# Kernel optimization log

Hardware: AMD Instinct MI355X
Metric: run time of the kernel (lower is better)

## Reference

```python
import jax, jax.numpy as jnp
import numpy as np

B, S, HID = 2, 2048, 2048
H, D_NOPE, D_ROPE, D_V, R = 16, 128, 64, 128, 512
D_Q = D_NOPE + D_ROPE  # 192
MAX_POS = 4096
EPS = 1e-6


def setup_inputs() -> dict:
    key = jax.random.key(0)
    ks = jax.random.split(key, 10)
    hidden_states = jax.random.normal(ks[0], (B, S, HID), dtype=jnp.float32)
    cos = jax.random.uniform(ks[1], (MAX_POS, D_ROPE // 2), dtype=jnp.float32)
    sin = jax.random.uniform(ks[2], (MAX_POS, D_ROPE // 2), dtype=jnp.float32)
    position_ids = jnp.arange(B * S, dtype=jnp.int64).reshape(B, S)
    sc = lambda d: 1.0 / np.sqrt(d)
    Wq = jax.random.normal(ks[3], (HID, H * D_Q), dtype=jnp.float32) * sc(HID)
    Wkv_a = jax.random.normal(ks[4], (HID, R + D_ROPE), dtype=jnp.float32) * sc(HID)
    ln_g = jnp.ones((R,), dtype=jnp.float32)
    ln_b = jnp.zeros((R,), dtype=jnp.float32)
    Wkv_b = jax.random.normal(ks[5], (R, H * (D_NOPE + D_V)), dtype=jnp.float32) * sc(R)
    Wo = jax.random.normal(ks[6], (H * D_V, HID), dtype=jnp.float32) * sc(H * D_V)
    return {"hidden_states": hidden_states, "cos": cos, "sin": sin,
            "position_ids": position_ids, "Wq": Wq, "Wkv_a": Wkv_a,
            "ln_g": ln_g, "ln_b": ln_b, "Wkv_b": Wkv_b, "Wo": Wo}


def _rope(t, cos, sin, position_ids):
    # t: [B,S,Hh,D_ROPE]; cos/sin: [MAX_POS, D_ROPE//2]
    c = cos[position_ids]  # [B,S,D_ROPE//2]
    s = sin[position_ids]
    c2 = jnp.concatenate([c, c], axis=-1)[:, :, None, :]  # [B,S,1,D_ROPE]
    s2 = jnp.concatenate([s, s], axis=-1)[:, :, None, :]
    half = t.shape[-1] // 2
    x1, x2 = t[..., :half], t[..., half:]
    rot = jnp.concatenate([-x2, x1], axis=-1)
    return t * c2 + rot * s2


def reference(hidden_states, cos, sin, position_ids, Wq, Wkv_a, ln_g, ln_b, Wkv_b, Wo):
    b, s, _ = hidden_states.shape
    # Q projection -> split nope/rope parts
    q = (hidden_states @ Wq).reshape(b, s, H, D_Q)
    q_nope, q_pe = q[..., :D_NOPE], q[..., D_NOPE:]
    q_pe = _rope(q_pe, cos, sin, position_ids)
    query = jnp.concatenate([q_nope, q_pe], axis=-1)  # [B,S,H,192]

    # KV latent projection
    ckv = hidden_states @ Wkv_a  # [B,S,R+D_ROPE]
    kv_c, k_pe = ckv[..., :R], ckv[..., R:]
    mu = jnp.mean(kv_c, axis=-1, keepdims=True)
    var = jnp.mean(jnp.square(kv_c - mu), axis=-1, keepdims=True)
    kv_c_n = (kv_c - mu) * jax.lax.rsqrt(var + EPS) * ln_g + ln_b
    k_pe = _rope(k_pe[:, :, None, :], cos, sin, position_ids)[:, :, 0, :]  # [B,S,64]

    # Expand latent -> per-head k_nope / v
    kv = (kv_c_n @ Wkv_b).reshape(b, s, H, D_NOPE + D_V)
    k_nope, v = kv[..., :D_NOPE], kv[..., D_NOPE:]
    key = jnp.concatenate(
        [k_nope, jnp.broadcast_to(k_pe[:, :, None, :], (b, s, H, D_ROPE))], axis=-1)

    scale = D_Q ** -0.5
    scores = jnp.einsum('bqhd,bkhd->bhqk', query, key) * scale
    causal = jnp.tril(jnp.ones((s, s), dtype=bool))
    scores = jnp.where(causal[None, None], scores, jnp.finfo(scores.dtype).min)
    attn = jax.nn.softmax(scores, axis=-1)
    out = jnp.einsum('bhqk,bkhd->bqhd', attn, v).reshape(b, s, H * D_V)
    return out @ Wo
```

## Files before the change

### kernel.cpp

```cpp
#include <hip/hip_runtime.h>
#include <math.h>
#include <stdint.h>

#define B_      2
#define S_      2048
#define HID_    2048
#define H_      16
#define D_NOPE_ 128
#define D_ROPE_ 64
#define D_V_    128
#define R_      512
#define D_Q_    192
#define NTOK    (B_ * S_)
#define EPS_    1e-6f

typedef __attribute__((ext_vector_type(8))) short bf16x8;
typedef __attribute__((ext_vector_type(4))) float f32x4;

__device__ __forceinline__ short f2bf(float x) {
    union { float f; unsigned u; } un; un.f = x;
    unsigned r = (un.u + 0x7fffu + ((un.u >> 16) & 1u)) >> 16;
    return (short)r;
}
__device__ __forceinline__ float bf2f(short s) {
    union { unsigned u; float f; } un;
    un.u = ((unsigned)(unsigned short)s) << 16;
    return un.f;
}

__device__ __forceinline__ void async_ld16(const short* gsrc, short* ldst) {
    __builtin_amdgcn_global_load_lds(
        (const __attribute__((address_space(1))) void*)gsrc,
        (__attribute__((address_space(3))) void*)ldst, 16, 0, 0);
}

#define BARX() { __builtin_amdgcn_sched_barrier(0); __builtin_amdgcn_s_barrier(); __builtin_amdgcn_sched_barrier(0); }

__device__ __forceinline__ void tc_body(const float* __restrict__ W,
                                        short* __restrict__ WT,
                                        int K, int Nreal, int bx, int by, int t) {
    __shared__ float T[32][33];
    const int n0 = bx * 32, k0 = by * 32;
    const int r = t >> 3, c4 = (t & 7) * 4;
    float4 v = make_float4(0.f, 0.f, 0.f, 0.f);
    if (n0 < Nreal) v = *(const float4*)&W[(size_t)(k0 + r) * Nreal + n0 + c4];
    T[r][c4 + 0] = v.x; T[r][c4 + 1] = v.y; T[r][c4 + 2] = v.z; T[r][c4 + 3] = v.w;
    __syncthreads();
    const int n = t >> 3, k4 = (t & 7) * 4;
    ushort4 o;
    o.x = (unsigned short)f2bf(T[k4 + 0][n]);
    o.y = (unsigned short)f2bf(T[k4 + 1][n]);
    o.z = (unsigned short)f2bf(T[k4 + 2][n]);
    o.w = (unsigned short)f2bf(T[k4 + 3][n]);
    *(ushort4*)&WT[(size_t)(n0 + n) * K + k0 + k4] = o;
}

__global__ __launch_bounds__(256) void prep(const float* __restrict__ hidden,
                                            short* __restrict__ hid_bf,
                                            const float* __restrict__ Wq,
                                            const float* __restrict__ Wkv_a,
                                            const float* __restrict__ Wkv_b,
                                            const float* __restrict__ Wo,
                                            short* __restrict__ WqkaT,
                                            short* __restrict__ WkbT,
                                            short* __restrict__ WoT) {
    const int bid = blockIdx.x, t = threadIdx.x;
    if (bid < 8192) {
        int i = bid * 256 + t;
        float4 v = ((const float4*)hidden)[i];
        ushort4 o;
        o.x = (unsigned short)f2bf(v.x); o.y = (unsigned short)f2bf(v.y);
        o.z = (unsigned short)f2bf(v.z); o.w = (unsigned short)f2bf(v.w);
        ((ushort4*)hid_bf)[i] = o;
    } else if (bid < 8192 + 6144) {
        int idx = bid - 8192;
        tc_body(Wq, WqkaT, 2048, 3072, idx % 96, idx / 96, t);
    } else if (bid < 8192 + 6144 + 1536) {
        int idx = bid - (8192 + 6144);
        tc_body(Wkv_a, WqkaT + (size_t)3072 * 2048, 2048, 576, idx % 24, idx / 24, t);
    } else if (bid < 8192 + 6144 + 1536 + 2048) {
        int idx = bid - (8192 + 6144 + 1536);
        tc_body(Wkv_b, WkbT, 512, 4096, idx % 128, idx / 128, t);
    } else {
        int idx = bid - (8192 + 6144 + 1536 + 2048);
        tc_body(Wo, WoT, 2048, 2048, idx % 64, idx / 64, t);
    }
}

template <int QA>
__global__ __launch_bounds__(512) void gemm8(const short* __restrict__ A,
                                             const short* __restrict__ BT,
                                             void* __restrict__ C0,
                                             float* __restrict__ C1,
                                             short* __restrict__ VtOut,
                                             const float* __restrict__ cosT,
                                             const float* __restrict__ sinT,
                                             const int* __restrict__ pid,
                                             int N, int K, int nbx) {
    __shared__ short LB[2][4][8192];

    const int tid = threadIdx.x, lane = tid & 63, w = tid >> 6;
    const int c16 = lane & 15, g = lane >> 4;
    const int wr = w >> 2, wc = w & 3;
    const int qph = (g ^ ((c16 >> 1) & 3)) * 8;

    const int nwg = gridDim.x;
    const int swz = (blockIdx.x & 7) * (nwg >> 3) + (blockIdx.x >> 3);
    const int brow = (swz / nbx) * 256, bcol = (swz % nbx) * 256;

    const int o0 = w * 1024 + lane * 16;
    const int o1 = o0 + 8192;
    const int r0 = o0 >> 6, lc0 = ((o0 >> 4) & 3) ^ ((r0 >> 1) & 3);
    const int r1 = o1 >> 6, lc1 = ((o1 >> 4) & 3) ^ ((r1 >> 1) & 3);
    const short* aS0 = A + (size_t)(brow + r0) * K + lc0 * 8;
    const short* aS1 = A + (size_t)(brow + r1) * K + lc1 * 8;
    const short* bS0 = BT + (size_t)(bcol + r0) * K + lc0 * 8;
    const short* bS1 = BT + (size_t)(bcol + r1) * K + lc1 * 8;
    const int d0 = w * 512, d1 = 4096 + w * 512;

    f32x4 zero = {0.f, 0.f, 0.f, 0.f};
    f32x4 acc[8][4];
#pragma unroll
    for (int i = 0; i < 8; ++i)
#pragma unroll
        for (int j = 0; j < 4; ++j) acc[i][j] = zero;

    const int NT = K >> 6;
    async_ld16(aS0,      &LB[0][0][d0]);  async_ld16(aS1,      &LB[0][0][d1]);
    async_ld16(aS0 + 32, &LB[0][1][d0]);  async_ld16(aS1 + 32, &LB[0][1][d1]);
    async_ld16(bS0,      &LB[0][2][d0]);  async_ld16(bS1,      &LB[0][2][d1]);
    async_ld16(bS0 + 32, &LB[0][3][d0]);  async_ld16(bS1 + 32, &LB[0][3][d1]);
    asm volatile("s_waitcnt vmcnt(0)" ::: "memory");
    BARX();

    int cur = 0;
    const int arb = wr * 128, brb = wc * 64;
    for (int kt = 0; kt < NT; ++kt) {
        const bool stg = (kt + 1 < NT);
        const int ko = (kt + 1) * 64;
        short (*CB)[8192] = LB[cur];
        short (*NB)[8192] = LB[cur ^ 1];
        bf16x8 af[4], bf[4];

#pragma unroll
        for (int ni = 0; ni < 4; ++ni)
            bf[ni] = *(const bf16x8*)&CB[2][(brb + ni * 16 + c16) * 32 + qph];
#pragma unroll
        for (int mi = 0; mi < 4; ++mi)
            af[mi] = *(const bf16x8*)&CB[0][(arb + mi * 16 + c16) * 32 + qph];
        if (stg) { async_ld16(aS0 + ko, &NB[0][d0]); async_ld16(aS1 + ko, &NB[0][d1]); }
        BARX();
        __builtin_amdgcn_s_setprio(1);
#pragma unroll
        for (int mi = 0; mi < 4; ++mi)
#pragma unroll
            for (int ni = 0; ni < 4; ++ni)
                acc[mi][ni] = __builtin_amdgcn_mfma_f32_16x16x32_bf16(af[mi], bf[ni], acc[mi][ni], 0, 0, 0);
        __builtin_amdgcn_s_setprio(0);
        BARX();

#pragma unroll
        for (int mi = 0; mi < 4; ++mi)
            af[mi] = *(const bf16x8*)&CB[0][(arb + 64 + mi * 16 + c16) * 32 + qph];
        if (stg) {
            async_ld16(bS0 + ko, &NB[2][d0]); async_ld16(bS1 + ko, &NB[2][d1]);
            asm volatile("s_waitcnt vmcnt(4)" ::: "memory");
        } else {
            asm volatile("s_waitcnt vmcnt(0)" ::: "memory");
        }
        BARX();
        __builtin_amdgcn_s_setprio(1);
#pragma unroll
        for (int mi = 0; mi < 4; ++mi)
#pragma unroll
            for (int ni = 0; ni < 4; ++ni)
                acc[4 + mi][ni] = __builtin_amdgcn_mfma_f32_16x16x32_bf16(af[mi], bf[ni], acc[4 + mi][ni], 0, 0, 0);
        __builtin_amdgcn_s_setprio(0);
        BARX();

#pragma unroll
        for (int ni = 0; ni < 4; ++ni)
            bf[ni] = *(const bf16x8*)&CB[3][(brb + ni * 16 + c16) * 32 + qph];
#pragma unroll
        for (int mi = 0; mi < 4; ++mi)
            af[mi] = *(const bf16x8*)&CB[1][(arb + mi * 16 + c16) * 32 + qph];
        if (stg) { async_ld16(aS0 + ko + 32, &NB[1][d0]); async_ld16(aS1 + ko + 32, &NB[1][d1]); }
        BARX();
        __builtin_amdgcn_s_setprio(1);
#pragma unroll
        for (int mi = 0; mi < 4; ++mi)
#pragma unroll
            for (int ni = 0; ni < 4; ++ni)
                acc[mi][ni] = __builtin_amdgcn_mfma_f32_16x16x32_bf16(af[mi], bf[ni], acc[mi][ni], 0, 0, 0);
        __builtin_amdgcn_s_setprio(0);
        BARX();

#pragma unroll
        for (int mi = 0; mi < 4; ++mi)
            af[mi] = *(const bf16x8*)&CB[1][(arb + 64 + mi * 16 + c16) * 32 + qph];
        if (stg) {
            async_ld16(bS0 + ko + 32, &NB[3][d0]); async_ld16(bS1 + ko + 32, &NB[3][d1]);
            asm volatile("s_waitcnt vmcnt(4)" ::: "memory");
        }
        BARX();
        __builtin_amdgcn_s_setprio(1);
#pragma unroll
        for (int mi = 0; mi < 4; ++mi)
#pragma unroll
            for (int ni = 0; ni < 4; ++ni)
                acc[4 + mi][ni] = __builtin_amdgcn_mfma_f32_16x16x32_bf16(af[mi], bf[ni], acc[4 + mi][ni], 0, 0, 0);
        __builtin_amdgcn_s_setprio(0);
        BARX();

        cur ^= 1;
    }

    if (QA) {
        const int wcol = bcol + wc * 64;
        if (wcol < 3072) {
            short* qb = (short*)C0;
            if ((wcol % 192) == 128) {
#pragma unroll
                for (int mi = 0; mi < 8; ++mi)
#pragma unroll
                    for (int reg = 0; reg < 4; ++reg) {
                        int row = brow + wr * 128 + mi * 16 + 4 * g + reg;
                        int pos = pid[row];
                        float cc1 = cosT[pos * 32 + c16],      ss1 = sinT[pos * 32 + c16];
                        float cc2 = cosT[pos * 32 + 16 + c16], ss2 = sinT[pos * 32 + 16 + c16];
                        float a0 = acc[mi][0][reg], a1 = acc[mi][1][reg];
                        float a2 = acc[mi][2][reg], a3 = acc[mi][3][reg];
                        size_t rb = (size_t)row * 3072 + wcol;
                        qb[rb + c16]      = f2bf(a0 * cc1 - a2 * ss1);
                        qb[rb + 16 + c16] = f2bf(a1 * cc2 - a3 * ss2);
                        qb[rb + 32 + c16] = f2bf(a2 * cc1 + a0 * ss1);
                        qb[rb + 48 + c16] = f2bf(a3 * cc2 + a1 * ss2);
                    }
            } else {
#pragma unroll
                for (int mi = 0; mi < 8; ++mi)
#pragma unroll
                    for (int ni = 0; ni < 4; ++ni)
#pragma unroll
                        for (int reg = 0; reg < 4; ++reg) {
                            int row = brow + wr * 128 + mi * 16 + 4 * g + reg;
                            qb[(size_t)row * 3072 + wcol + ni * 16 + c16] = f2bf(acc[mi][ni][reg]);
                        }
            }
        } else if (wcol < 3712) {
#pragma unroll
            for (int mi = 0; mi < 8; ++mi)
#pragma unroll
                for (int ni = 0; ni < 4; ++ni)
#pragma unroll
                    for (int reg = 0; reg < 4; ++reg) {
                        int row = brow + wr * 128 + mi * 16 + 4 * g + reg;
                        int col = wcol - 3072 + ni * 16 + c16;
                        C1[(size_t)row * 640 + col] = acc[mi][ni][reg];
                    }
        }
    } else {
        short* cc = (short*)C0;
        short* LT = &LB[0][0][0];
        const int wcol = bcol + wc * 64;
        if (wc < 2) {
#pragma unroll
            for (int mi = 0; mi < 8; ++mi)
#pragma unroll
                for (int ni = 0; ni < 4; ++ni)
#pragma unroll
                    for (int reg = 0; reg < 4; ++reg) {
                        int row = brow + wr * 128 + mi * 16 + 4 * g + reg;
                        cc[(size_t)row * N + wcol + ni * 16 + c16] = f2bf(acc[mi][ni][reg]);
                    }
        } else {
#pragma unroll
            for (int mi = 0; mi < 8; ++mi)
#pragma unroll
                for (int ni = 0; ni < 4; ++ni)
#pragma unroll
                    for (int reg = 0; reg < 4; ++reg) {
                        int d = wc * 64 - 128 + ni * 16 + c16;
                        int s = wr * 128 + mi * 16 + 4 * g + reg;
                        LT[d * 256 + (s ^ ((d & 15) << 3))] = f2bf(acc[mi][ni][reg]);
                    }
        }
        __syncthreads();
        const int bb = brow >> 11, hh = bcol >> 8, sbase = brow & 2047;
#pragma unroll
        for (int j = 0; j < 8; ++j) {
            int d = j * 16 + (tid >> 5);
            int s0 = (tid & 31) * 8;
            bf16x8 v = *(const bf16x8*)&LT[d * 256 + (s0 ^ ((d & 15) << 3))];
            *(bf16x8*)&VtOut[((size_t)((bb * 16 + hh) * 128 + d)) * 2048 + sbase + s0] = v;
        }
    }
}

__global__ __launch_bounds__(512) void gemm8n(const short* __restrict__ A,
                                              const short* __restrict__ BT,
                                              float* __restrict__ C,
                                              int N, int K, int nbx) {
    __shared__ short LA[2][2][4096];
    __shared__ short LBt[2][2][8192];

    const int tid = threadIdx.x, lane = tid & 63, w = tid >> 6;
    const int c16 = lane & 15, g = lane >> 4;
    const int wr = w >> 2, wc = w & 3;
    const int qph = (g ^ ((c16 >> 1) & 3)) * 8;

    const int nwg = gridDim.x;
    const int swz = (blockIdx.x & 7) * (nwg >> 3) + (blockIdx.x >> 3);
    const int brow = (swz / nbx) * 128, bcol = (swz % nbx) * 256;

    const int oA = tid * 16;
    const int rA = oA >> 6, lcA = ((oA >> 4) & 3) ^ ((rA >> 1) & 3);
    const short* aS = A + (size_t)(brow + rA) * K + lcA * 8;
    const int dA = oA >> 1;

    const int o0 = w * 1024 + lane * 16, o1 = o0 + 8192;
    const int r0 = o0 >> 6, lc0 = ((o0 >> 4) & 3) ^ ((r0 >> 1) & 3);
    const int r1 = o1 >> 6, lc1 = ((o1 >> 4) & 3) ^ ((r1 >> 1) & 3);
    const short* bS0 = BT + (size_t)(bcol + r0) * K + lc0 * 8;
    const short* bS1 = BT + (size_t)(bcol + r1) * K + lc1 * 8;
    const int d0 = o0 >> 1, d1 = o1 >> 1;

    f32x4 zero = {0.f, 0.f, 0.f, 0.f};
    f32x4 acc[4][4];
#pragma unroll
    for (int i = 0; i < 4; ++i)
#pragma unroll
        for (int j = 0; j < 4; ++j) acc[i][j] = zero;

    const int NT = K >> 6;
    async_ld16(aS,      &LA[0][0][dA]);
    async_ld16(aS + 32, &LA[0][1][dA]);
    async_ld16(bS0,      &LBt[0][0][d0]); async_ld16(bS1,      &LBt[0][0][d1]);
    async_ld16(bS0 + 32, &LBt[0][1][d0]); async_ld16(bS1 + 32, &LBt[0][1][d1]);
    asm volatile("s_waitcnt vmcnt(0)" ::: "memory");
    BARX();

    int cur = 0;
    const int arb = wr * 64, brb = wc * 64;
    for (int kt = 0; kt < NT; ++kt) {
        const bool stg = (kt + 1 < NT);
        const int ko = (kt + 1) * 64;
        bf16x8 af[4], bf[4];

#pragma unroll
        for (int mi = 0; mi < 4; ++mi)
            af[mi] = *(const bf16x8*)&LA[cur][0][(arb + mi * 16 + c16) * 32 + qph];
#pragma unroll
        for (int ni = 0; ni < 4; ++ni)
            bf[ni] = *(const bf16x8*)&LBt[cur][0][(brb + ni * 16 + c16) * 32 + qph];
        if (stg) {
            async_ld16(aS + ko, &LA[cur ^ 1][0][dA]);
            async_ld16(bS0 + ko, &LBt[cur ^ 1][0][d0]);
            async_ld16(bS1 + ko, &LBt[cur ^ 1][0][d1]);
            asm volatile("s_waitcnt vmcnt(3)" ::: "memory");
        } else {
            asm volatile("s_waitcnt vmcnt(0)" ::: "memory");
        }
        BARX();
        __builtin_amdgcn_s_setprio(1);
#pragma unroll
        for (int mi = 0; mi < 4; ++mi)
#pragma unroll
            for (int ni = 0; ni < 4; ++ni)
                acc[mi][ni] = __builtin_amdgcn_mfma_f32_16x16x32_bf16(af[mi], bf[ni], acc[mi][ni], 0, 0, 0);
        __builtin_amdgcn_s_setprio(0);
        BARX();

#pragma unroll
        for (int mi = 0; mi < 4; ++mi)
            af[mi] = *(const bf16x8*)&LA[cur][1][(arb + mi * 16 + c16) * 32 + qph];
#pragma unroll
        for (int ni = 0; ni < 4; ++ni)
            bf[ni] = *(const bf16x8*)&LBt[cur][1][(brb + ni * 16 + c16) * 32 + qph];
        if (stg) {
            async_ld16(aS + ko + 32, &LA[cur ^ 1][1][dA]);
            async_ld16(bS0 + ko + 32, &LBt[cur ^ 1][1][d0]);
            async_ld16(bS1 + ko + 32, &LBt[cur ^ 1][1][d1]);
            asm volatile("s_waitcnt vmcnt(3)" ::: "memory");
        }
        BARX();
        __builtin_amdgcn_s_setprio(1);
#pragma unroll
        for (int mi = 0; mi < 4; ++mi)
#pragma unroll
            for (int ni = 0; ni < 4; ++ni)
                acc[mi][ni] = __builtin_amdgcn_mfma_f32_16x16x32_bf16(af[mi], bf[ni], acc[mi][ni], 0, 0, 0);
        __builtin_amdgcn_s_setprio(0);
        BARX();

        cur ^= 1;
    }

#pragma unroll
    for (int mi = 0; mi < 4; ++mi)
#pragma unroll
        for (int ni = 0; ni < 4; ++ni)
#pragma unroll
            for (int reg = 0; reg < 4; ++reg) {
                int row = brow + wr * 64 + mi * 16 + 4 * g + reg;
                int col = bcol + wc * 64 + ni * 16 + c16;
                C[(size_t)row * N + col] = acc[mi][ni][reg];
            }
}

__global__ __launch_bounds__(256) void ln_rope(const float* __restrict__ ckv,
                                               const float* __restrict__ gam,
                                               const float* __restrict__ bet,
                                               const float* __restrict__ cosT,
                                               const float* __restrict__ sinT,
                                               const int* __restrict__ pid,
                                               short* __restrict__ kvcn,
                                               short* __restrict__ kpe) {
    const int tok = blockIdx.x, tid = threadIdx.x;
    const float* x = ckv + (size_t)tok * 640;
    float v0 = x[tid], v1 = x[tid + 256];
    float s = v0 + v1, sq = v0 * v0 + v1 * v1;
#pragma unroll
    for (int m = 1; m < 64; m <<= 1) { s += __shfl_xor(s, m); sq += __shfl_xor(sq, m); }
    __shared__ float ws[8];
    int wid = tid >> 6, lane = tid & 63;
    if (lane == 0) { ws[wid] = s; ws[4 + wid] = sq; }
    __syncthreads();
    s = ws[0] + ws[1] + ws[2] + ws[3];
    sq = ws[4] + ws[5] + ws[6] + ws[7];
    float mean = s * (1.f / 512.f);
    float var = sq * (1.f / 512.f) - mean * mean;
    float rstd = rsqrtf(var + EPS_);
    kvcn[(size_t)tok * 512 + tid]       = f2bf((v0 - mean) * rstd * gam[tid] + bet[tid]);
    kvcn[(size_t)tok * 512 + tid + 256] = f2bf((v1 - mean) * rstd * gam[tid + 256] + bet[tid + 256]);
    if (tid < 32) {
        int pos = pid[tok];
        float c = cosT[pos * 32 + tid], sn = sinT[pos * 32 + tid];
        float x1 = x[512 + tid], x2 = x[512 + 32 + tid];
        kpe[(size_t)tok * 64 + tid]      = f2bf(x1 * c - x2 * sn);
        kpe[(size_t)tok * 64 + 32 + tid] = f2bf(x2 * c + x1 * sn);
    }
}

__global__ __launch_bounds__(256) void flash_mfma(const short* __restrict__ qb,
                                                  const short* __restrict__ kvb,
                                                  const short* __restrict__ kpe,
                                                  const short* __restrict__ Vt,
                                                  short* __restrict__ attno) {
    __shared__ short Ks[2][64 * 128];
    __shared__ short Vs[2][128 * 64];
    __shared__ short P[4][16][72];

    const int flat = blockIdx.x;
    const int xcd = flat & 7, idx = flat >> 3;
    const int bh = xcd + 8 * (idx >> 4);
    const int pair = idx & 15;
    const int b = bh >> 4, h = bh & 15;

    const int tid = threadIdx.x, lane = tid & 63, w = tid >> 6;
    const int c16 = lane & 15, g = lane >> 4, g8 = g * 8;
    const float SC2 = 0.10412063f;

    const int o = w * 1024 + lane * 16;
    const int rK = o >> 8, ccK = ((o >> 4) & 15) ^ (rK & 7);
    const int rV = o >> 7, ccV = ((o >> 4) & 7) ^ (rV & 7);
    const short* kB0  = kvb + ((size_t)((b * 2048 + rK) * 16 + h)) * 256 + ccK * 8;
    const short* vB0  = Vt + ((size_t)((b * 16 + h) * 128 + rV)) * 2048 + ccV * 8;
    const short* peB0 = kpe + (size_t)(b * 2048 + c16) * 64 + g8;

    f32x4 zero = {0.f, 0.f, 0.f, 0.f};

#define STAGE(BUF)                                                                  \
    {                                                                               \
        _Pragma("unroll")                                                           \
        for (int rnd = 0; rnd < 4; ++rnd)                                           \
            async_ld16(kRun + (size_t)rnd * 65536,                                  \
                       &Ks[BUF][(rnd * 4096 + w * 1024) >> 1]);                     \
        _Pragma("unroll")                                                           \
        for (int rnd = 0; rnd < 4; ++rnd)                                           \
            async_ld16(vRun + (size_t)rnd * 65536,                                  \
                       &Vs[BUF][(rnd * 4096 + w * 1024) >> 1]);                     \
        kRun += 64 * 4096;                                                          \
        vRun += 64;                                                                 \
    }

    for (int half = 0; half < 2; ++half) {
        const int qt = half ? (31 - pair) : pair;
        const int q0 = qt * 64;
        const int qrow = q0 + w * 16;

        const size_t qbase = ((size_t)(b * 2048 + qrow + c16) * 16 + h) * 192 + g8;
        bf16x8 qf[6];
#pragma unroll
        for (int ks = 0; ks < 6; ++ks) qf[ks] = *(const bf16x8*)(qb + qbase + 32 * ks);

        f32x4 acc[8];
#pragma unroll
        for (int i = 0; i < 8; ++i) acc[i] = zero;
        float mreg = -INFINITY;
        float lreg = 0.f;

        const short* kRun = kB0;
        const short* vRun = vB0;
        const short* peRun = peB0;

        const int nt = qt + 1;
        STAGE(0);
        __syncthreads();
        int cur = 0;

        for (int kt = 0; kt < nt; ++kt) {
            if (kt + 1 < nt) STAGE(cur ^ 1);

            f32x4 sc[4];
#pragma unroll
            for (int i = 0; i < 4; ++i) sc[i] = zero;

            __builtin_amdgcn_s_setprio(1);
#pragma unroll
            for (int ks = 0; ks < 4; ++ks)
#pragma unroll
                for (int nb = 0; nb < 4; ++nb) {
                    int row = nb * 16 + c16;
                    bf16x8 kf = *(const bf16x8*)&Ks[cur][row * 128 + (((g + 4 * ks) ^ (row & 7)) << 3)];
                    sc[nb] = __builtin_amdgcn_mfma_f32_16x16x32_bf16(kf, qf[ks], sc[nb], 0, 0, 0);
                }
#pragma unroll
            for (int ks = 0; ks < 2; ++ks)
#pragma unroll
                for (int nb = 0; nb < 4; ++nb) {
                    bf16x8 kf = *(const bf16x8*)(peRun + (size_t)nb * 16 * 64 + ks * 32);
                    sc[nb] = __builtin_amdgcn_mfma_f32_16x16x32_bf16(kf, qf[4 + ks], sc[nb], 0, 0, 0);
                }
            __builtin_amdgcn_s_setprio(0);
            peRun += 64 * 64;

            if (kt == nt - 1) {
#pragma unroll
                for (int nb = 0; nb < 4; ++nb)
#pragma unroll
                    for (int reg = 0; reg < 4; ++reg)
                        if (nb * 16 + 4 * g + reg > w * 16 + c16) sc[nb][reg] = -INFINITY;
            }

            float m01 = fmaxf(fmaxf(sc[0][0], sc[0][1]), fmaxf(sc[0][2], sc[0][3]));
            float m23 = fmaxf(fmaxf(sc[1][0], sc[1][1]), fmaxf(sc[1][2], sc[1][3]));
            float m45 = fmaxf(fmaxf(sc[2][0], sc[2][1]), fmaxf(sc[2][2], sc[2][3]));
            float m67 = fmaxf(fmaxf(sc[3][0], sc[3][1]), fmaxf(sc[3][2], sc[3][3]));
            float rmax = fmaxf(fmaxf(m01, m23), fmaxf(m45, m67));
            rmax = fmaxf(rmax, __shfl_xor(rmax, 16));
            rmax = fmaxf(rmax, __shfl_xor(rmax, 32));

            if (__any(rmax * SC2 - mreg > 8.f)) {
                float mnew = fmaxf(mreg, rmax * SC2);
                float alpha = exp2f(mreg - mnew);
                mreg = mnew;
                lreg *= alpha;
                float ar[4];
#pragma unroll
                for (int reg = 0; reg < 4; ++reg) ar[reg] = __shfl(alpha, 4 * g + reg);
#pragma unroll
                for (int nb = 0; nb < 8; ++nb)
#pragma unroll
                    for (int reg = 0; reg < 4; ++reg) acc[nb][reg] *= ar[reg];
            }

#pragma unroll
            for (int nb = 0; nb < 4; ++nb) {
                float p0 = exp2f(fmaf(sc[nb][0], SC2, -mreg));
                float p1 = exp2f(fmaf(sc[nb][1], SC2, -mreg));
                float p2 = exp2f(fmaf(sc[nb][2], SC2, -mreg));
                float p3 = exp2f(fmaf(sc[nb][3], SC2, -mreg));
                lreg += (p0 + p1) + (p2 + p3);
                short* pr = &P[w][c16][nb * 16 + 4 * g];
                pr[0] = f2bf(p0); pr[1] = f2bf(p1); pr[2] = f2bf(p2); pr[3] = f2bf(p3);
            }

            __builtin_amdgcn_s_setprio(1);
#pragma unroll
            for (int ks = 0; ks < 2; ++ks) {
                bf16x8 pf = *(const bf16x8*)&P[w][c16][ks * 32 + g8];
#pragma unroll
                for (int nb = 0; nb < 8; ++nb) {
                    int row = nb * 16 + c16;
                    bf16x8 vf = *(const bf16x8*)&Vs[cur][row * 64 + (((g + 4 * ks) ^ (row & 7)) << 3)];
                    acc[nb] = __builtin_amdgcn_mfma_f32_16x16x32_bf16(pf, vf, acc[nb], 0, 0, 0);
                }
            }
            __builtin_amdgcn_s_setprio(0);

            __syncthreads();
            cur ^= 1;
        }

        lreg += __shfl_xor(lreg, 16);
        lreg += __shfl_xor(lreg, 32);
        float linv[4];
#pragma unroll
        for (int reg = 0; reg < 4; ++reg) linv[reg] = 1.f / __shfl(lreg, 4 * g + reg);
#pragma unroll
        for (int nb = 0; nb < 8; ++nb)
#pragma unroll
            for (int reg = 0; reg < 4; ++reg)
                attno[((size_t)(b * 2048 + qrow + 4 * g + reg) * 16 + h) * 128 + nb * 16 + c16] =
                    f2bf(acc[nb][reg] * linv[reg]);
    }
#undef STAGE
}

extern "C" void kernel_launch(void* const* d_in, const int* in_sizes, int n_in,
                              void* d_out, int out_size, void* d_ws, size_t ws_size,
                              hipStream_t stream) {
    const float* hidden = (const float*)d_in[0];
    const float* cosT   = (const float*)d_in[1];
    const float* sinT   = (const float*)d_in[2];
    const int*   pid    = (const int*)d_in[3];
    const float* Wq     = (const float*)d_in[4];
    const float* Wkv_a  = (const float*)d_in[5];
    const float* ln_g   = (const float*)d_in[6];
    const float* ln_b   = (const float*)d_in[7];
    const float* Wkv_b  = (const float*)d_in[8];
    const float* Wo     = (const float*)d_in[9];
    float* out = (float*)d_out;

    char* p = (char*)d_ws;
    short* hid_bf = (short*)p;               p += (size_t)NTOK * 2048 * 2;
    short* WqkaT  = (short*)p;               p += (size_t)3840 * 2048 * 2;
    short* WkbT   = (short*)p;               p += (size_t)4096 * 512 * 2;
    short* WoT    = (short*)p;               p += (size_t)2048 * 2048 * 2;
    char*  big    = p;                       p += (size_t)NTOK * 3072 * 4;
    short* qbuf   = (short*)p;               p += (size_t)NTOK * 3072 * 2;
    short* kvcn   = (short*)p;               p += (size_t)NTOK * 512 * 2;
    short* kpe    = (short*)p;               p += (size_t)NTOK * 64 * 2;
    short* kvb    = (short*)p;               p += (size_t)NTOK * 4096 * 2;

    float* ckv   = (float*)big;
    short* Vt    = (short*)(big + (size_t)NTOK * 640 * 4);
    short* attno = (short*)(big + (size_t)NTOK * 640 * 4 + (size_t)2 * 16 * 128 * 2048 * 2);

    prep<<<22016, 256, 0, stream>>>(hidden, hid_bf, Wq, Wkv_a, Wkv_b, Wo, WqkaT, WkbT, WoT);
    gemm8<1><<<240, 512, 0, stream>>>(hid_bf, WqkaT, qbuf, ckv, nullptr,
                                      cosT, sinT, pid, 3840, 2048, 15);
    ln_rope<<<NTOK, 256, 0, stream>>>(ckv, ln_g, ln_b, cosT, sinT, pid, kvcn, kpe);
    gemm8<0><<<256, 512, 0, stream>>>(kvcn, WkbT, kvb, nullptr, Vt,
                                      nullptr, nullptr, nullptr, 4096, 512, 16);
    flash_mfma<<<512, 256, 0, stream>>>(qbuf, kvb, kpe, Vt, attno);
    gemm8n<<<256, 512, 0, stream>>>(attno, WoT, out, 2048, 2048, 8);
}
```

Measured before the change: 274.4 us.

## Single-buffer flash attention LDS with split K/V staging and one q-tile per block

The flash attention kernel drops double-buffered K/V shared memory in favour of single buffers. K for the next tile is staged right after the QK^T phase and V after the PV phase, with extra barriers between them. Each block now handles one 64-row query tile (1024 blocks, heaviest tiles first) instead of a balanced pair of tiles. Launch bounds request 3 blocks per CU. The goal is higher occupancy and better latency hiding, at the cost of less load/compute overlap inside a block and more per-block setup.

```diff
diff --git a/kernel.cpp b/kernel.cpp
--- a/kernel.cpp
+++ b/kernel.cpp
@@ -442,20 +442,21 @@
     }
 }
 
-__global__ __launch_bounds__(256) void flash_mfma(const short* __restrict__ qb,
-                                                  const short* __restrict__ kvb,
-                                                  const short* __restrict__ kpe,
-                                                  const short* __restrict__ Vt,
-                                                  short* __restrict__ attno) {
-    __shared__ short Ks[2][64 * 128];
-    __shared__ short Vs[2][128 * 64];
+__global__ __launch_bounds__(256, 3) void flash_mfma(const short* __restrict__ qb,
+                                                     const short* __restrict__ kvb,
+                                                     const short* __restrict__ kpe,
+                                                     const short* __restrict__ Vt,
+                                                     short* __restrict__ attno) {
+    __shared__ short Ks[64 * 128];
+    __shared__ short Vs[128 * 64];
     __shared__ short P[4][16][72];
 
     const int flat = blockIdx.x;
     const int xcd = flat & 7, idx = flat >> 3;
-    const int bh = xcd + 8 * (idx >> 4);
-    const int pair = idx & 15;
+    const int bh = xcd + 8 * (idx >> 5);
+    const int qt = 31 - (idx & 31);
     const int b = bh >> 4, h = bh & 15;
+    const int q0 = qt * 64;
 
     const int tid = threadIdx.x, lane = tid & 63, w = tid >> 6;
     const int c16 = lane & 15, g = lane >> 4, g8 = g * 8;
@@ -464,148 +465,145 @@
     const int o = w * 1024 + lane * 16;
     const int rK = o >> 8, ccK = ((o >> 4) & 15) ^ (rK & 7);
     const int rV = o >> 7, ccV = ((o >> 4) & 7) ^ (rV & 7);
-    const short* kB0  = kvb + ((size_t)((b * 2048 + rK) * 16 + h)) * 256 + ccK * 8;
-    const short* vB0  = Vt + ((size_t)((b * 16 + h) * 128 + rV)) * 2048 + ccV * 8;
-    const short* peB0 = kpe + (size_t)(b * 2048 + c16) * 64 + g8;
+    const short* kRun = kvb + ((size_t)((b * 2048 + rK) * 16 + h)) * 256 + ccK * 8;
+    const short* vRun = Vt + ((size_t)((b * 16 + h) * 128 + rV)) * 2048 + ccV * 8;
+    const short* peRun = kpe + (size_t)(b * 2048 + c16) * 64 + g8;
+
+    const int qrow = q0 + w * 16;
+    const size_t qbase = ((size_t)(b * 2048 + qrow + c16) * 16 + h) * 192 + g8;
+    bf16x8 qf[6];
+#pragma unroll
+    for (int ks = 0; ks < 6; ++ks) qf[ks] = *(const bf16x8*)(qb + qbase + 32 * ks);
 
     f32x4 zero = {0.f, 0.f, 0.f, 0.f};
-
-#define STAGE(BUF)                                                                  \
+    f32x4 acc[8];
+#pragma unroll
+    for (int i = 0; i < 8; ++i) acc[i] = zero;
+    float mreg = -INFINITY;
+    float lreg = 0.f;
+
+#define STAGE_K()                                                                   \
     {                                                                               \
         _Pragma("unroll")                                                           \
         for (int rnd = 0; rnd < 4; ++rnd)                                           \
             async_ld16(kRun + (size_t)rnd * 65536,                                  \
-                       &Ks[BUF][(rnd * 4096 + w * 1024) >> 1]);                     \
+                       &Ks[(rnd * 4096 + w * 1024) >> 1]);                          \
+        kRun += 64 * 4096;                                                          \
+    }
+#define STAGE_V()                                                                   \
+    {                                                                               \
         _Pragma("unroll")                                                           \
         for (int rnd = 0; rnd < 4; ++rnd)                                           \
             async_ld16(vRun + (size_t)rnd * 65536,                                  \
-                       &Vs[BUF][(rnd * 4096 + w * 1024) >> 1]);                     \
-        kRun += 64 * 4096;                                                          \
+                       &Vs[(rnd * 4096 + w * 1024) >> 1]);                          \
         vRun += 64;                                                                 \
     }
 
-    for (int half = 0; half < 2; ++half) {
-        const int qt = half ? (31 - pair) : pair;
-        const int q0 = qt * 64;
-        const int qrow = q0 + w * 16;
-
-        const size_t qbase = ((size_t)(b * 2048 + qrow + c16) * 16 + h) * 192 + g8;
-        bf16x8 qf[6];
-#pragma unroll
-        for (int ks = 0; ks < 6; ++ks) qf[ks] = *(const bf16x8*)(qb + qbase + 32 * ks);
-
-        f32x4 acc[8];
-#pragma unroll
-        for (int i = 0; i < 8; ++i) acc[i] = zero;
-        float mreg = -INFINITY;
-        float lreg = 0.f;
-
-        const short* kRun = kB0;
-        const short* vRun = vB0;
-        const short* peRun = peB0;
-
-        const int nt = qt + 1;
-        STAGE(0);
+    const int nt = qt + 1;
+    STAGE_K();
+    STAGE_V();
+    __syncthreads();
+
+    for (int kt = 0; kt < nt; ++kt) {
+        const bool stg = (kt + 1 < nt);
+
+        f32x4 sc[4];
+#pragma unroll
+        for (int i = 0; i < 4; ++i) sc[i] = zero;
+
+        __builtin_amdgcn_s_setprio(1);
+#pragma unroll
+        for (int ks = 0; ks < 4; ++ks)
+#pragma unroll
+            for (int nb = 0; nb < 4; ++nb) {
+                int row = nb * 16 + c16;
+                bf16x8 kf = *(const bf16x8*)&Ks[row * 128 + (((g + 4 * ks) ^ (row & 7)) << 3)];
+                sc[nb] = __builtin_amdgcn_mfma_f32_16x16x32_bf16(kf, qf[ks], sc[nb], 0, 0, 0);
+            }
+#pragma unroll
+        for (int ks = 0; ks < 2; ++ks)
+#pragma unroll
+            for (int nb = 0; nb < 4; ++nb) {
+                bf16x8 kf = *(const bf16x8*)(peRun + (size_t)nb * 16 * 64 + ks * 32);
+                sc[nb] = __builtin_amdgcn_mfma_f32_16x16x32_bf16(kf, qf[4 + ks], sc[nb], 0, 0, 0);
+            }
+        __builtin_amdgcn_s_setprio(0);
+        peRun += 64 * 64;
+
         __syncthreads();
-        int cur = 0;
-
-        for (int kt = 0; kt < nt; ++kt) {
-            if (kt + 1 < nt) STAGE(cur ^ 1);
-
-            f32x4 sc[4];
-#pragma unroll
-            for (int i = 0; i < 4; ++i) sc[i] = zero;
-
-            __builtin_amdgcn_s_setprio(1);
-#pragma unroll
-            for (int ks = 0; ks < 4; ++ks)
-#pragma unroll
-                for (int nb = 0; nb < 4; ++nb) {
-                    int row = nb * 16 + c16;
-                    bf16x8 kf = *(const bf16x8*)&Ks[cur][row * 128 + (((g + 4 * ks) ^ (row & 7)) << 3)];
-                    sc[nb] = __builtin_amdgcn_mfma_f32_16x16x32_bf16(kf, qf[ks], sc[nb], 0, 0, 0);
-                }
-#pragma unroll
-            for (int ks = 0; ks < 2; ++ks)
-#pragma unroll
-                for (int nb = 0; nb < 4; ++nb) {
-                    bf16x8 kf = *(const bf16x8*)(peRun + (size_t)nb * 16 * 64 + ks * 32);
-                    sc[nb] = __builtin_amdgcn_mfma_f32_16x16x32_bf16(kf, qf[4 + ks], sc[nb], 0, 0, 0);
-                }
-            __builtin_amdgcn_s_setprio(0);
-            peRun += 64 * 64;
-
-            if (kt == nt - 1) {
-#pragma unroll
-                for (int nb = 0; nb < 4; ++nb)
-#pragma unroll
-                    for (int reg = 0; reg < 4; ++reg)
-                        if (nb * 16 + 4 * g + reg > w * 16 + c16) sc[nb][reg] = -INFINITY;
+        if (stg) STAGE_K();
+
+        if (kt == nt - 1) {
+#pragma unroll
+            for (int nb = 0; nb < 4; ++nb)
+#pragma unroll
+                for (int reg = 0; reg < 4; ++reg)
+                    if (nb * 16 + 4 * g + reg > w * 16 + c16) sc[nb][reg] = -INFINITY;
+        }
+
+        float m01 = fmaxf(fmaxf(sc[0][0], sc[0][1]), fmaxf(sc[0][2], sc[0][3]));
+        float m23 = fmaxf(fmaxf(sc[1][0], sc[1][1]), fmaxf(sc[1][2], sc[1][3]));
+        float m45 = fmaxf(fmaxf(sc[2][0], sc[2][1]), fmaxf(sc[2][2], sc[2][3]));
+        float m67 = fmaxf(fmaxf(sc[3][0], sc[3][1]), fmaxf(sc[3][2], sc[3][3]));
+        float rmax = fmaxf(fmaxf(m01, m23), fmaxf(m45, m67));
+        rmax = fmaxf(rmax, __shfl_xor(rmax, 16));
+        rmax = fmaxf(rmax, __shfl_xor(rmax, 32));
+
+        if (__any(rmax * SC2 - mreg > 8.f)) {
+            float mnew = fmaxf(mreg, rmax * SC2);
+            float alpha = exp2f(mreg - mnew);
+            mreg = mnew;
+            lreg *= alpha;
+            float ar[4];
+#pragma unroll
+            for (int reg = 0; reg < 4; ++reg) ar[reg] = __shfl(alpha, 4 * g + reg);
+#pragma unroll
+            for (int nb = 0; nb < 8; ++nb)
+#pragma unroll
+                for (int reg = 0; reg < 4; ++reg) acc[nb][reg] *= ar[reg];
+        }
+
+#pragma unroll
+        for (int nb = 0; nb < 4; ++nb) {
+            float p0 = exp2f(fmaf(sc[nb][0], SC2, -mreg));
+            float p1 = exp2f(fmaf(sc[nb][1], SC2, -mreg));
+            float p2 = exp2f(fmaf(sc[nb][2], SC2, -mreg));
+            float p3 = exp2f(fmaf(sc[nb][3], SC2, -mreg));
+            lreg += (p0 + p1) + (p2 + p3);
+            short* pr = &P[w][c16][nb * 16 + 4 * g];
+            pr[0] = f2bf(p0); pr[1] = f2bf(p1); pr[2] = f2bf(p2); pr[3] = f2bf(p3);
+        }
+
+        __builtin_amdgcn_s_setprio(1);
+#pragma unroll
+        for (int ks = 0; ks < 2; ++ks) {
+            bf16x8 pf = *(const bf16x8*)&P[w][c16][ks * 32 + g8];
+#pragma unroll
+            for (int nb = 0; nb < 8; ++nb) {
+                int row = nb * 16 + c16;
+                bf16x8 vf = *(const bf16x8*)&Vs[row * 64 + (((g + 4 * ks) ^ (row & 7)) << 3)];
+                acc[nb] = __builtin_amdgcn_mfma_f32_16x16x32_bf16(pf, vf, acc[nb], 0, 0, 0);
             }
-
-            float m01 = fmaxf(fmaxf(sc[0][0], sc[0][1]), fmaxf(sc[0][2], sc[0][3]));
-            float m23 = fmaxf(fmaxf(sc[1][0], sc[1][1]), fmaxf(sc[1][2], sc[1][3]));
-            float m45 = fmaxf(fmaxf(sc[2][0], sc[2][1]), fmaxf(sc[2][2], sc[2][3]));
-            float m67 = fmaxf(fmaxf(sc[3][0], sc[3][1]), fmaxf(sc[3][2], sc[3][3]));
-            float rmax = fmaxf(fmaxf(m01, m23), fmaxf(m45, m67));
-            rmax = fmaxf(rmax, __shfl_xor(rmax, 16));
-            rmax = fmaxf(rmax, __shfl_xor(rmax, 32));
-
-            if (__any(rmax * SC2 - mreg > 8.f)) {
-                float mnew = fmaxf(mreg, rmax * SC2);
-                float alpha = exp2f(mreg - mnew);
-                mreg = mnew;
-                lreg *= alpha;
-                float ar[4];
-#pragma unroll
-                for (int reg = 0; reg < 4; ++reg) ar[reg] = __shfl(alpha, 4 * g + reg);
-#pragma unroll
-                for (int nb = 0; nb < 8; ++nb)
-#pragma unroll
-                    for (int reg = 0; reg < 4; ++reg) acc[nb][reg] *= ar[reg];
-            }
-
-#pragma unroll
-            for (int nb = 0; nb < 4; ++nb) {
-                float p0 = exp2f(fmaf(sc[nb][0], SC2, -mreg));
-                float p1 = exp2f(fmaf(sc[nb][1], SC2, -mreg));
-                float p2 = exp2f(fmaf(sc[nb][2], SC2, -mreg));
-                float p3 = exp2f(fmaf(sc[nb][3], SC2, -mreg));
-                lreg += (p0 + p1) + (p2 + p3);
-                short* pr = &P[w][c16][nb * 16 + 4 * g];
-                pr[0] = f2bf(p0); pr[1] = f2bf(p1); pr[2] = f2bf(p2); pr[3] = f2bf(p3);
-            }
-
-            __builtin_amdgcn_s_setprio(1);
-#pragma unroll
-            for (int ks = 0; ks < 2; ++ks) {
-                bf16x8 pf = *(const bf16x8*)&P[w][c16][ks * 32 + g8];
-#pragma unroll
-                for (int nb = 0; nb < 8; ++nb) {
-                    int row = nb * 16 + c16;
-                    bf16x8 vf = *(const bf16x8*)&Vs[cur][row * 64 + (((g + 4 * ks) ^ (row & 7)) << 3)];
-                    acc[nb] = __builtin_amdgcn_mfma_f32_16x16x32_bf16(pf, vf, acc[nb], 0, 0, 0);
-                }
-            }
-            __builtin_amdgcn_s_setprio(0);
-
-            __syncthreads();
-            cur ^= 1;
-        }
-
-        lreg += __shfl_xor(lreg, 16);
-        lreg += __shfl_xor(lreg, 32);
-        float linv[4];
-#pragma unroll
-        for (int reg = 0; reg < 4; ++reg) linv[reg] = 1.f / __shfl(lreg, 4 * g + reg);
-#pragma unroll
-        for (int nb = 0; nb < 8; ++nb)
-#pragma unroll
-            for (int reg = 0; reg < 4; ++reg)
-                attno[((size_t)(b * 2048 + qrow + 4 * g + reg) * 16 + h) * 128 + nb * 16 + c16] =
-                    f2bf(acc[nb][reg] * linv[reg]);
-    }
-#undef STAGE
+        }
+        __builtin_amdgcn_s_setprio(0);
+
+        __syncthreads();
+        if (stg) STAGE_V();
+    }
+#undef STAGE_K
+#undef STAGE_V
+
+    lreg += __shfl_xor(lreg, 16);
+    lreg += __shfl_xor(lreg, 32);
+    float linv[4];
+#pragma unroll
+    for (int reg = 0; reg < 4; ++reg) linv[reg] = 1.f / __shfl(lreg, 4 * g + reg);
+#pragma unroll
+    for (int nb = 0; nb < 8; ++nb)
+#pragma unroll
+        for (int reg = 0; reg < 4; ++reg)
+            attno[((size_t)(b * 2048 + qrow + 4 * g + reg) * 16 + h) * 128 + nb * 16 + c16] =
+                f2bf(acc[nb][reg] * linv[reg]);
 }
 
 extern "C" void kernel_launch(void* const* d_in, const int* in_sizes, int n_in,
@@ -644,6 +642,6 @@
     ln_rope<<<NTOK, 256, 0, stream>>>(ckv, ln_g, ln_b, cosT, sinT, pid, kvcn, kpe);
     gemm8<0><<<256, 512, 0, stream>>>(kvcn, WkbT, kvb, nullptr, Vt,
                                       nullptr, nullptr, nullptr, 4096, 512, 16);
-    flash_mfma<<<512, 256, 0, stream>>>(qbuf, kvb, kpe, Vt, attno);
+    flash_mfma<<<1024, 256, 0, stream>>>(qbuf, kvb, kpe, Vt, attno);
     gemm8n<<<256, 512, 0, stream>>>(attno, WoT, out, 2048, 2048, 8);
 }
```

Measured after the change: 294.9 us. 1.07x slower.

## Process paired causal query tiles together to share K/V tile loads

Applied to the files above, without the earlier changes.

Each flash-attention block previously ran its two query tiles (pair and 31-pair) one after the other, streaming the K/V tiles through LDS twice. The kernel now keeps both tiles' Q fragments, accumulators and softmax state live at once. Each staged K/V tile therefore feeds both tiles until the shorter one finishes, and the longer tile then continues alone. The block-to-(batch, head, pair) mapping is also reordered so paired blocks use mirrored pair indices. The cost is roughly doubled accumulator and Q register use, which may reduce occupancy or cause spills.

```diff
diff --git a/kernel.cpp b/kernel.cpp
--- a/kernel.cpp
+++ b/kernel.cpp
@@ -452,10 +452,14 @@
     __shared__ short P[4][16][72];
 
     const int flat = blockIdx.x;
-    const int xcd = flat & 7, idx = flat >> 3;
-    const int bh = xcd + 8 * (idx >> 4);
-    const int pair = idx & 15;
+    const int hs = flat >> 8, rr = flat & 255;
+    const int xcd = rr & 7, idx = rr >> 3;
+    const int bh = xcd + 8 * (idx >> 3);
+    const int ps = idx & 7;
+    const int pair = hs ? (15 - ps) : ps;
     const int b = bh >> 4, h = bh & 15;
+    const int qtA = pair, qtB = 31 - pair;
+    const int ntA = qtA + 1, ntB = qtB + 1;
 
     const int tid = threadIdx.x, lane = tid & 63, w = tid >> 6;
     const int c16 = lane & 15, g = lane >> 4, g8 = g * 8;
@@ -464,11 +468,30 @@
     const int o = w * 1024 + lane * 16;
     const int rK = o >> 8, ccK = ((o >> 4) & 15) ^ (rK & 7);
     const int rV = o >> 7, ccV = ((o >> 4) & 7) ^ (rV & 7);
-    const short* kB0  = kvb + ((size_t)((b * 2048 + rK) * 16 + h)) * 256 + ccK * 8;
-    const short* vB0  = Vt + ((size_t)((b * 16 + h) * 128 + rV)) * 2048 + ccV * 8;
-    const short* peB0 = kpe + (size_t)(b * 2048 + c16) * 64 + g8;
+    const short* kRun = kvb + ((size_t)((b * 2048 + rK) * 16 + h)) * 256 + ccK * 8;
+    const short* vRun = Vt + ((size_t)((b * 16 + h) * 128 + rV)) * 2048 + ccV * 8;
+    const short* peRun = kpe + (size_t)(b * 2048 + c16) * 64 + g8;
+
+    const int qrowA = qtA * 64 + w * 16;
+    const int qrowB = qtB * 64 + w * 16;
+    bf16x8 qfA[6], qfB[6];
+    {
+        const size_t qa = ((size_t)(b * 2048 + qrowA + c16) * 16 + h) * 192 + g8;
+        const size_t qbb = ((size_t)(b * 2048 + qrowB + c16) * 16 + h) * 192 + g8;
+#pragma unroll
+        for (int ks = 0; ks < 6; ++ks) {
+            qfA[ks] = *(const bf16x8*)(qb + qa + 32 * ks);
+            qfB[ks] = *(const bf16x8*)(qb + qbb + 32 * ks);
+        }
+    }
 
     f32x4 zero = {0.f, 0.f, 0.f, 0.f};
+    f32x4 accA[8], accB[8];
+#pragma unroll
+    for (int i = 0; i < 8; ++i) { accA[i] = zero; accB[i] = zero; }
+    float mA = -INFINITY, lA = 0.f;
+    float mB = -INFINITY, lB = 0.f;
+    int cur = 0;
 
 #define STAGE(BUF)                                                                  \
     {                                                                               \
@@ -484,115 +507,63 @@
         vRun += 64;                                                                 \
     }
 
-    for (int half = 0; half < 2; ++half) {
-        const int qt = half ? (31 - pair) : pair;
-        const int q0 = qt * 64;
-        const int qrow = q0 + w * 16;
-
-        const size_t qbase = ((size_t)(b * 2048 + qrow + c16) * 16 + h) * 192 + g8;
-        bf16x8 qf[6];
-#pragma unroll
-        for (int ks = 0; ks < 6; ++ks) qf[ks] = *(const bf16x8*)(qb + qbase + 32 * ks);
-
-        f32x4 acc[8];
-#pragma unroll
-        for (int i = 0; i < 8; ++i) acc[i] = zero;
-        float mreg = -INFINITY;
-        float lreg = 0.f;
-
-        const short* kRun = kB0;
-        const short* vRun = vB0;
-        const short* peRun = peB0;
-
-        const int nt = qt + 1;
-        STAGE(0);
-        __syncthreads();
-        int cur = 0;
-
-        for (int kt = 0; kt < nt; ++kt) {
-            if (kt + 1 < nt) STAGE(cur ^ 1);
-
-            f32x4 sc[4];
-#pragma unroll
-            for (int i = 0; i < 4; ++i) sc[i] = zero;
-
-            __builtin_amdgcn_s_setprio(1);
-#pragma unroll
-            for (int ks = 0; ks < 4; ++ks)
-#pragma unroll
-                for (int nb = 0; nb < 4; ++nb) {
-                    int row = nb * 16 + c16;
-                    bf16x8 kf = *(const bf16x8*)&Ks[cur][row * 128 + (((g + 4 * ks) ^ (row & 7)) << 3)];
-                    sc[nb] = __builtin_amdgcn_mfma_f32_16x16x32_bf16(kf, qf[ks], sc[nb], 0, 0, 0);
-                }
-#pragma unroll
-            for (int ks = 0; ks < 2; ++ks)
-#pragma unroll
-                for (int nb = 0; nb < 4; ++nb) {
-                    bf16x8 kf = *(const bf16x8*)(peRun + (size_t)nb * 16 * 64 + ks * 32);
-                    sc[nb] = __builtin_amdgcn_mfma_f32_16x16x32_bf16(kf, qf[4 + ks], sc[nb], 0, 0, 0);
-                }
-            __builtin_amdgcn_s_setprio(0);
-            peRun += 64 * 64;
-
-            if (kt == nt - 1) {
-#pragma unroll
-                for (int nb = 0; nb < 4; ++nb)
-#pragma unroll
-                    for (int reg = 0; reg < 4; ++reg)
-                        if (nb * 16 + 4 * g + reg > w * 16 + c16) sc[nb][reg] = -INFINITY;
+    auto softpv = [&](f32x4 (&sc)[4], f32x4 (&acc)[8], float& mreg, float& lreg,
+                      bool domask) {
+        if (domask) {
+#pragma unroll
+            for (int nb = 0; nb < 4; ++nb)
+#pragma unroll
+                for (int reg = 0; reg < 4; ++reg)
+                    if (nb * 16 + 4 * g + reg > w * 16 + c16) sc[nb][reg] = -INFINITY;
+        }
+        float m01 = fmaxf(fmaxf(sc[0][0], sc[0][1]), fmaxf(sc[0][2], sc[0][3]));
+        float m23 = fmaxf(fmaxf(sc[1][0], sc[1][1]), fmaxf(sc[1][2], sc[1][3]));
+        float m45 = fmaxf(fmaxf(sc[2][0], sc[2][1]), fmaxf(sc[2][2], sc[2][3]));
+        float m67 = fmaxf(fmaxf(sc[3][0], sc[3][1]), fmaxf(sc[3][2], sc[3][3]));
+        float rmax = fmaxf(fmaxf(m01, m23), fmaxf(m45, m67));
+        rmax = fmaxf(rmax, __shfl_xor(rmax, 16));
+        rmax = fmaxf(rmax, __shfl_xor(rmax, 32));
+
+        if (__any(rmax * SC2 - mreg > 8.f)) {
+            float mnew = fmaxf(mreg, rmax * SC2);
+            float alpha = exp2f(mreg - mnew);
+            mreg = mnew;
+            lreg *= alpha;
+            float ar[4];
+#pragma unroll
+            for (int reg = 0; reg < 4; ++reg) ar[reg] = __shfl(alpha, 4 * g + reg);
+#pragma unroll
+            for (int nb = 0; nb < 8; ++nb)
+#pragma unroll
+                for (int reg = 0; reg < 4; ++reg) acc[nb][reg] *= ar[reg];
+        }
+
+#pragma unroll
+        for (int nb = 0; nb < 4; ++nb) {
+            float p0 = exp2f(fmaf(sc[nb][0], SC2, -mreg));
+            float p1 = exp2f(fmaf(sc[nb][1], SC2, -mreg));
+            float p2 = exp2f(fmaf(sc[nb][2], SC2, -mreg));
+            float p3 = exp2f(fmaf(sc[nb][3], SC2, -mreg));
+            lreg += (p0 + p1) + (p2 + p3);
+            short* pr = &P[w][c16][nb * 16 + 4 * g];
+            pr[0] = f2bf(p0); pr[1] = f2bf(p1); pr[2] = f2bf(p2); pr[3] = f2bf(p3);
+        }
+
+        __builtin_amdgcn_s_setprio(1);
+#pragma unroll
+        for (int ks = 0; ks < 2; ++ks) {
+            bf16x8 pf = *(const bf16x8*)&P[w][c16][ks * 32 + g8];
+#pragma unroll
+            for (int nb = 0; nb < 8; ++nb) {
+                int row = nb * 16 + c16;
+                bf16x8 vf = *(const bf16x8*)&Vs[cur][row * 64 + (((g + 4 * ks) ^ (row & 7)) << 3)];
+                acc[nb] = __builtin_amdgcn_mfma_f32_16x16x32_bf16(pf, vf, acc[nb], 0, 0, 0);
             }
-
-            float m01 = fmaxf(fmaxf(sc[0][0], sc[0][1]), fmaxf(sc[0][2], sc[0][3]));
-            float m23 = fmaxf(fmaxf(sc[1][0], sc[1][1]), fmaxf(sc[1][2], sc[1][3]));
-            float m45 = fmaxf(fmaxf(sc[2][0], sc[2][1]), fmaxf(sc[2][2], sc[2][3]));
-            float m67 = fmaxf(fmaxf(sc[3][0], sc[3][1]), fmaxf(sc[3][2], sc[3][3]));
-            float rmax = fmaxf(fmaxf(m01, m23), fmaxf(m45, m67));
-            rmax = fmaxf(rmax, __shfl_xor(rmax, 16));
-            rmax = fmaxf(rmax, __shfl_xor(rmax, 32));
-
-            if (__any(rmax * SC2 - mreg > 8.f)) {
-                float mnew = fmaxf(mreg, rmax * SC2);
-                float alpha = exp2f(mreg - mnew);
-                mreg = mnew;
-                lreg *= alpha;
-                float ar[4];
-#pragma unroll
-                for (int reg = 0; reg < 4; ++reg) ar[reg] = __shfl(alpha, 4 * g + reg);
-#pragma unroll
-                for (int nb = 0; nb < 8; ++nb)
-#pragma unroll
-                    for (int reg = 0; reg < 4; ++reg) acc[nb][reg] *= ar[reg];
-            }
-
-#pragma unroll
-            for (int nb = 0; nb < 4; ++nb) {
-                float p0 = exp2f(fmaf(sc[nb][0], SC2, -mreg));
-                float p1 = exp2f(fmaf(sc[nb][1], SC2, -mreg));
-                float p2 = exp2f(fmaf(sc[nb][2], SC2, -mreg));
-                float p3 = exp2f(fmaf(sc[nb][3], SC2, -mreg));
-                lreg += (p0 + p1) + (p2 + p3);
-                short* pr = &P[w][c16][nb * 16 + 4 * g];
-                pr[0] = f2bf(p0); pr[1] = f2bf(p1); pr[2] = f2bf(p2); pr[3] = f2bf(p3);
-            }
-
-            __builtin_amdgcn_s_setprio(1);
-#pragma unroll
-            for (int ks = 0; ks < 2; ++ks) {
-                bf16x8 pf = *(const bf16x8*)&P[w][c16][ks * 32 + g8];
-#pragma unroll
-                for (int nb = 0; nb < 8; ++nb) {
-                    int row = nb * 16 + c16;
-                    bf16x8 vf = *(const bf16x8*)&Vs[cur][row * 64 + (((g + 4 * ks) ^ (row & 7)) << 3)];
-                    acc[nb] = __builtin_amdgcn_mfma_f32_16x16x32_bf16(pf, vf, acc[nb], 0, 0, 0);
-                }
-            }
-            __builtin_amdgcn_s_setprio(0);
-
-            __syncthreads();
-            cur ^= 1;
-        }
-
+        }
+        __builtin_amdgcn_s_setprio(0);
+    };
+
+    auto epi = [&](f32x4 (&acc)[8], float lreg, int qrow) {
         lreg += __shfl_xor(lreg, 16);
         lreg += __shfl_xor(lreg, 32);
         float linv[4];
@@ -604,7 +575,81 @@
             for (int reg = 0; reg < 4; ++reg)
                 attno[((size_t)(b * 2048 + qrow + 4 * g + reg) * 16 + h) * 128 + nb * 16 + c16] =
                     f2bf(acc[nb][reg] * linv[reg]);
-    }
+    };
+
+    STAGE(0);
+    __syncthreads();
+
+    for (int kt = 0; kt < ntA; ++kt) {
+        STAGE(cur ^ 1);
+
+        f32x4 scA[4], scB[4];
+#pragma unroll
+        for (int i = 0; i < 4; ++i) { scA[i] = zero; scB[i] = zero; }
+
+        __builtin_amdgcn_s_setprio(1);
+#pragma unroll
+        for (int ks = 0; ks < 4; ++ks)
+#pragma unroll
+            for (int nb = 0; nb < 4; ++nb) {
+                int row = nb * 16 + c16;
+                bf16x8 kf = *(const bf16x8*)&Ks[cur][row * 128 + (((g + 4 * ks) ^ (row & 7)) << 3)];
+                scA[nb] = __builtin_amdgcn_mfma_f32_16x16x32_bf16(kf, qfA[ks], scA[nb], 0, 0, 0);
+                scB[nb] = __builtin_amdgcn_mfma_f32_16x16x32_bf16(kf, qfB[ks], scB[nb], 0, 0, 0);
+            }
+#pragma unroll
+        for (int ks = 0; ks < 2; ++ks)
+#pragma unroll
+            for (int nb = 0; nb < 4; ++nb) {
+                bf16x8 kf = *(const bf16x8*)(peRun + (size_t)nb * 16 * 64 + ks * 32);
+                scA[nb] = __builtin_amdgcn_mfma_f32_16x16x32_bf16(kf, qfA[4 + ks], scA[nb], 0, 0, 0);
+                scB[nb] = __builtin_amdgcn_mfma_f32_16x16x32_bf16(kf, qfB[4 + ks], scB[nb], 0, 0, 0);
+            }
+        __builtin_amdgcn_s_setprio(0);
+        peRun += 64 * 64;
+
+        softpv(scA, accA, mA, lA, kt == ntA - 1);
+        softpv(scB, accB, mB, lB, false);
+
+        __syncthreads();
+        cur ^= 1;
+    }
+
+    epi(accA, lA, qrowA);
+
+    for (int kt = ntA; kt < ntB; ++kt) {
+        if (kt + 1 < ntB) STAGE(cur ^ 1);
+
+        f32x4 scB[4];
+#pragma unroll
+        for (int i = 0; i < 4; ++i) scB[i] = zero;
+
+        __builtin_amdgcn_s_setprio(1);
+#pragma unroll
+        for (int ks = 0; ks < 4; ++ks)
+#pragma unroll
+            for (int nb = 0; nb < 4; ++nb) {
+                int row = nb * 16 + c16;
+                bf16x8 kf = *(const bf16x8*)&Ks[cur][row * 128 + (((g + 4 * ks) ^ (row & 7)) << 3)];
+                scB[nb] = __builtin_amdgcn_mfma_f32_16x16x32_bf16(kf, qfB[ks], scB[nb], 0, 0, 0);
+            }
+#pragma unroll
+        for (int ks = 0; ks < 2; ++ks)
+#pragma unroll
+            for (int nb = 0; nb < 4; ++nb) {
+                bf16x8 kf = *(const bf16x8*)(peRun + (size_t)nb * 16 * 64 + ks * 32);
+                scB[nb] = __builtin_amdgcn_mfma_f32_16x16x32_bf16(kf, qfB[4 + ks], scB[nb], 0, 0, 0);
+            }
+        __builtin_amdgcn_s_setprio(0);
+        peRun += 64 * 64;
+
+        softpv(scB, accB, mB, lB, kt == ntB - 1);
+
+        __syncthreads();
+        cur ^= 1;
+    }
+
+    epi(accB, lB, qrowB);
 #undef STAGE
 }
 
```

Measured after the change: 327.4 us. +19.3%, slower.
